# Kernel tuning notes

Hardware: AMD Instinct MI355X
Metric: run time of the kernel (lower is better)

## Reference

```python
import jax, jax.numpy as jnp
import numpy as np

SIGMAS = (1.0, 10.0, 100.0, 1000.0)
EPS_RATIO = 1e-3  # lambda ridge term and ratio clip epsilon


def euclidsq(x, y):
    # squared pairwise Euclidean distances, [m, n]
    d = jnp.sum(x * x, axis=-1)[:, None] + jnp.sum(y * y, axis=-1)[None, :] - 2.0 * (x @ y.T)
    return jnp.maximum(d, 0.0)


def kmm_ratio(Kdede, Kdenu, lam):
    # original: inv(Kdede + lam*I) @ Kdenu @ ones == solve(A, Kdenu @ ones)
    n_de = Kdede.shape[0]
    A = Kdede + lam * jnp.eye(n_de, dtype=Kdede.dtype)
    B = jnp.sum(Kdenu, axis=1, keepdims=True)  # [n_de, 1]
    return jnp.linalg.solve(A, B)


def estimate_ratio(x_de, x_nu):
    # averaged KMM ratio over Gaussian kernels with fixed sigmas, then clip
    dsq_dede = euclidsq(x_de, x_de)
    dsq_denu = euclidsq(x_de, x_nu)
    ratio = 0.0
    for s in SIGMAS:
        inv2s2 = 1.0 / (2.0 * s * s)
        Kdede = jnp.exp(-dsq_dede * inv2s2)
        Kdenu = jnp.exp(-dsq_denu * inv2s2)
        ratio = ratio + kmm_ratio(Kdede, Kdenu, EPS_RATIO)
    ratio = ratio / len(SIGMAS)
    return jax.nn.relu(ratio) + EPS_RATIO  # clip_ratio=True


def reference(z1, z2, perm1, perm2):
    n, d = z1.shape
    z1s, z2s = z1[perm1], z2[perm2]
    # numerator ratio over full concatenated embeddings
    num_ratio = estimate_ratio(jnp.concatenate([z1, z2], axis=-1),
                               jnp.concatenate([z1s, z2s], axis=-1))
    num_ratio = 1.0 / num_ratio  # [n, 1]
    x_nu = jnp.concatenate([z2, z2], axis=-1)  # constant across samples

    def per_sample(z1_i):
        # x_de row j = concat(z1_i, z2_shuffled[j])
        x_de = jnp.concatenate([jnp.broadcast_to(z1_i, (n, d)), z2s], axis=-1)
        return jnp.sum(estimate_ratio(x_de, x_nu))

    denum_sums = jax.vmap(per_sample)(z1)  # [n]
    loss = jnp.sum(-jnp.log(num_ratio[:, 0] / denum_sums))
    return loss


def setup_inputs() -> dict:
    key = jax.random.key(0)
    k1, k2 = jax.random.split(key)
    n, d = 256, 128
    z1 = jax.random.normal(k1, (n, d), dtype=jnp.float32)
    z2 = jax.random.normal(k2, (n, d), dtype=jnp.float32)
    perm1 = jnp.arange(n, dtype=jnp.int32)
    perm2 = jnp.arange(n, dtype=jnp.int32)
    return {"z1": z1, "z2": z2, "perm1": perm1, "perm2": perm2}
```

## Files before the change

### kernel.cpp

```cpp
#include <hip/hip_runtime.h>
#include <math.h>

#define N 256
#define Dd 128

__device__ __forceinline__ double inv2s2_of(int s){
    return (s==0)?0.5:(s==1)?5.0e-3:(s==2)?5.0e-5:5.0e-7;
}

__device__ __forceinline__ void sweep32(double P[32][33], int tid){
    if (tid < 64){
        int r = tid & 31, cg = tid >> 5;
        for (int j = 0; j < 32; j++){
            double d    = P[j][j];
            double invd = 1.0 / d;
            double cr   = P[r][j];
            double s    = cr * invd;
            bool rj = (r == j);
            double nv[16];
            #pragma unroll
            for (int c = 0; c < 16; c++){
                int col = cg*16 + c;
                double pj = P[j][col];
                double v  = P[r][col];
                nv[c] = rj ? ((col == j) ? -invd : v * invd)
                           : ((col == j) ? s : v - s*pj);
            }
            #pragma unroll
            for (int c = 0; c < 16; c++) P[r][cg*16+c] = nv[c];
        }
        #pragma unroll
        for (int c = 0; c < 16; c++) P[r][cg*16+c] = -P[r][cg*16+c];
    }
}

__global__ void k_dist(const float* __restrict__ z1, const float* __restrict__ z2,
                       const int* __restrict__ p1, const int* __restrict__ p2,
                       double* __restrict__ S0, float* __restrict__ M4,
                       float* __restrict__ U4, double* __restrict__ bpart){
    __shared__ float Xs[16][17], Ys[16][17];
    int w = blockIdx.z;
    int tx = threadIdx.x, ty = threadIdx.y;
    int row = blockIdx.y*16 + ty, col = blockIdx.x*16 + tx;
    const float *Xb[2], *Yb[2]; const int *Xp[2], *Yp[2]; int npair = 1;
    Xb[1]=0; Yb[1]=0; Xp[0]=0; Yp[0]=0; Xp[1]=0; Yp[1]=0;
    switch(w){
        case 0: Xb[0]=z1; Yb[0]=z1; Xb[1]=z2; Yb[1]=z2; npair=2; break;
        case 1: Xb[0]=z1; Yb[0]=z1; Yp[0]=p1; Xb[1]=z2; Yb[1]=z2; Yp[1]=p2; npair=2; break;
        case 2: Xb[0]=z2; Yb[0]=z2; Xp[0]=p2; Yp[0]=p2; break;
        case 3: Xb[0]=z2; Yb[0]=z2; Xp[0]=p2; break;
        default:Xb[0]=z1; Yb[0]=z2; break;
    }
    double acc = 0.0;
    for (int p = 0; p < npair; p++){
        const float* X = Xb[p]; const float* Y = Yb[p];
        int xr = blockIdx.y*16 + ty; if (Xp[p]) xr = Xp[p][xr];
        int yr = blockIdx.x*16 + ty; if (Yp[p]) yr = Yp[p][yr];
        for (int c = 0; c < Dd; c += 16){
            __syncthreads();
            Xs[ty][tx] = X[xr*Dd + c + tx];
            Ys[ty][tx] = Y[yr*Dd + c + tx];
            __syncthreads();
            #pragma unroll
            for (int t = 0; t < 16; t++){
                float d = Xs[ty][t] - Ys[tx][t];
                acc += (double)d * (double)d;
            }
        }
    }
    int o = row*N + col;
    if (w == 0){
        #pragma unroll
        for (int s = 0; s < 4; s++){
            double v = exp(-inv2s2_of(s)*acc);
            if (row == col) v += 1.0e-3;
            S0[(size_t)(4+s)*N*N + o] = v;
        }
    } else if (w == 1){
        #pragma unroll
        for (int s = 0; s < 4; s++){
            double v = exp(-inv2s2_of(s)*acc);
            v += __shfl_down(v, 8, 16);
            v += __shfl_down(v, 4, 16);
            v += __shfl_down(v, 2, 16);
            v += __shfl_down(v, 1, 16);
            if (tx == 0) bpart[((size_t)s*N + row)*16 + blockIdx.x] = v;
        }
    } else if (w == 2){
        #pragma unroll
        for (int s = 0; s < 4; s++){
            double v = exp(-inv2s2_of(s)*acc);
            if (row == col) v += 1.0e-3;
            S0[(size_t)s*N*N + o] = v;
        }
    } else if (w == 3){
        #pragma unroll
        for (int s = 0; s < 4; s++) M4[s*N*N + o] = (float)exp(-inv2s2_of(s)*acc);
    } else {
        #pragma unroll
        for (int s = 0; s < 4; s++) U4[s*N*N + o] = (float)exp(-inv2s2_of(s)*acc);
    }
}

__global__ void k_gemm_nt(const float* __restrict__ M4, const float* __restrict__ U4,
                          double* __restrict__ Bmat, const double* __restrict__ S0,
                          double* __restrict__ Pg0, double* __restrict__ dsum){
    __shared__ float Ms[32][33], Us[32][33];
    __shared__ double P[32][33];
    int tx = threadIdx.x, ty = threadIdx.y;
    int tid = ty*16 + tx;
    if (blockIdx.z == 4){
        if (blockIdx.y != 0) return;
        int mat = blockIdx.x;
        if (mat == 0) dsum[tid] = 0.0;
        const double* S = S0 + (size_t)mat*65536;
        #pragma unroll
        for (int l = 0; l < 4; l++){
            int e = tid + l*256; P[e>>5][e&31] = S[(size_t)(e>>5)*N + (e&31)];
        }
        __syncthreads();
        sweep32(P, tid);
        __syncthreads();
        double* Pp = Pg0 + (size_t)mat*1024;
        #pragma unroll
        for (int l = 0; l < 4; l++){
            int e = tid + l*256; Pp[e] = P[e>>5][e&31];
        }
        return;
    }
    int s = blockIdx.z;
    const float* Mp = M4 + s*N*N;
    const float* Up = U4 + s*N*N;
    double* Bp = Bmat + s*N*N;
    int bj = blockIdx.y*32, bi = blockIdx.x*32;
    double a00=0, a01=0, a10=0, a11=0;
    for (int kc = 0; kc < N; kc += 32){
        __syncthreads();
        #pragma unroll
        for (int l = 0; l < 4; l++){
            int e = tid + l*256; int r = e >> 5, c = e & 31;
            Ms[r][c] = Mp[(bj+r)*N + kc + c];
            Us[r][c] = Up[(bi+r)*N + kc + c];
        }
        __syncthreads();
        #pragma unroll
        for (int k = 0; k < 32; k++){
            float x0 = Ms[2*ty][k], x1 = Ms[2*ty+1][k];
            float y0 = Us[2*tx][k], y1 = Us[2*tx+1][k];
            a00 += (double)x0*y0; a01 += (double)x0*y1;
            a10 += (double)x1*y0; a11 += (double)x1*y1;
        }
    }
    Bp[(bj+2*ty  )*N + bi+2*tx  ] = a00;
    Bp[(bj+2*ty  )*N + bi+2*tx+1] = a01;
    Bp[(bj+2*ty+1)*N + bi+2*tx  ] = a10;
    Bp[(bj+2*ty+1)*N + bi+2*tx+1] = a11;
}

__global__ void k_step(const double* __restrict__ Ssrc, double* __restrict__ Sdst,
                       const double* __restrict__ PgS, double* __restrict__ PgD, int k){
    __shared__ double Pl[32][33], EJ[32][33], Cl[32][33], El[32][33];
    int b = blockIdx.x;
    int mat = b & 7;
    int bx = b >> 3;
    const double* S = Ssrc + (size_t)mat*65536;
    double* D = Sdst + (size_t)mat*65536;
    const double* Pp = PgS + (size_t)mat*1024;
    int tid = threadIdx.x;
    int Kb = k*32;
    #pragma unroll
    for (int l = 0; l < 4; l++){
        int e = tid + l*256; Pl[e>>5][e&31] = Pp[e];
    }
    if (bx < 49){
        int I = bx / 7, J = bx % 7;
        int GI = ((I < k) ? I : I + 1) * 32;
        int GJ = ((J < k) ? J : J + 1) * 32;
        #pragma unroll
        for (int l = 0; l < 4; l++){
            int e = tid + l*256; int r = e >> 5, c = e & 31;
            El[r][c] = S[(size_t)(GI + r)*N + Kb + c];
            EJ[r][c] = S[(size_t)(GJ + r)*N + Kb + c];
        }
        __syncthreads();
        #pragma unroll
        for (int l = 0; l < 4; l++){
            int e = tid + l*256; int r = e >> 5, c = e & 31;
            double acc = 0.0;
            #pragma unroll
            for (int kk = 0; kk < 32; kk++) acc += EJ[r][kk] * Pl[kk][c];
            Cl[r][c] = acc;
        }
        __syncthreads();
        int pr = tid >> 4, pc = tid & 15;
        int r0 = 2*pr, c0 = 2*pc;
        double a00 = S[(size_t)(GI+r0)*N + GJ+c0];
        double a01 = S[(size_t)(GI+r0)*N + GJ+c0+1];
        double a10 = S[(size_t)(GI+r0+1)*N + GJ+c0];
        double a11 = S[(size_t)(GI+r0+1)*N + GJ+c0+1];
        #pragma unroll
        for (int kk = 0; kk < 32; kk++){
            double e0 = El[r0][kk],   e1 = El[r0+1][kk];
            double b0 = Cl[c0][kk],   b1 = Cl[c0+1][kk];
            a00 -= e0*b0; a01 -= e0*b1;
            a10 -= e1*b0; a11 -= e1*b1;
        }
        double* Dp = D + (size_t)(GI + r0)*N + GJ + c0;
        Dp[0]   = a00; Dp[1]   = a01;
        Dp[N]   = a10; Dp[N+1] = a11;
        if (I == k && J == k && k < 7){
            __syncthreads();
            El[r0][c0]   = a00; El[r0][c0+1]   = a01;
            El[r0+1][c0] = a10; El[r0+1][c0+1] = a11;
            __syncthreads();
            sweep32(El, tid);
            __syncthreads();
            double* Pd = PgD + (size_t)mat*1024;
            #pragma unroll
            for (int l = 0; l < 4; l++){
                int e = tid + l*256; Pd[e] = El[e>>5][e&31];
            }
        }
    } else {
        int T = bx - 49;
        int GT = ((T < k) ? T : T + 1) * 32;
        #pragma unroll
        for (int l = 0; l < 4; l++){
            int e = tid + l*256; int r = e >> 5, c = e & 31;
            El[r][c] = S[(size_t)(GT + r)*N + Kb + c];
        }
        __syncthreads();
        #pragma unroll
        for (int l = 0; l < 4; l++){
            int e = tid + l*256; int r = e >> 5, c = e & 31;
            double acc = 0.0;
            #pragma unroll
            for (int kk = 0; kk < 32; kk++) acc += El[r][kk] * Pl[kk][c];
            Cl[r][c] = acc;
        }
        __syncthreads();
        #pragma unroll
        for (int l = 0; l < 4; l++){
            int e = tid + l*256; int r = e >> 5, c = e & 31;
            D[(size_t)(GT + r)*N + Kb + c] = Cl[r][c];
        }
        #pragma unroll
        for (int l = 0; l < 4; l++){
            int e = tid + l*256; int cc = e >> 5, rr = e & 31;
            D[(size_t)(Kb + cc)*N + GT + rr] = Cl[rr][cc];
        }
        if (T == 0){
            #pragma unroll
            for (int l = 0; l < 4; l++){
                int e = tid + l*256; int i = e >> 5, j = e & 31;
                D[(size_t)(Kb + i)*N + Kb + j] = -Pl[i][j];
            }
        }
    }
}

__global__ void k_x(const double* __restrict__ Sfin, const double* __restrict__ Bmat,
                    float* __restrict__ Xm){
    int s = blockIdx.z;
    const double* Sp = Sfin + (size_t)s*N*N;
    const double* Bp = Bmat + (size_t)s*N*N;
    float* Xp = Xm + (size_t)s*N*N;
    __shared__ double Gs[32][33], Bs[32][33];
    int tx = threadIdx.x, ty = threadIdx.y;
    int tid = ty*16 + tx;
    int bj = blockIdx.y*32, bi = blockIdx.x*32;
    double a00=0, a01=0, a10=0, a11=0;
    for (int kc = 0; kc < N; kc += 32){
        __syncthreads();
        #pragma unroll
        for (int l = 0; l < 4; l++){
            int e = tid + l*256; int r = e >> 5, c = e & 31;
            Gs[r][c] = -Sp[(size_t)(bj+r)*N + kc + c];
            Bs[r][c] = Bp[(size_t)(kc+r)*N + bi + c];
        }
        __syncthreads();
        #pragma unroll
        for (int k = 0; k < 32; k++){
            double x0 = Gs[2*ty][k], x1 = Gs[2*ty+1][k];
            double y0 = Bs[k][2*tx], y1 = Bs[k][2*tx+1];
            a00 += x0*y0; a01 += x0*y1;
            a10 += x1*y0; a11 += x1*y1;
        }
    }
    Xp[(bj+2*ty  )*N + bi+2*tx  ] = (float)a00;
    Xp[(bj+2*ty  )*N + bi+2*tx+1] = (float)a01;
    Xp[(bj+2*ty+1)*N + bi+2*tx  ] = (float)a10;
    Xp[(bj+2*ty+1)*N + bi+2*tx+1] = (float)a11;
}

__global__ void k_red(const float* __restrict__ Xm, const double* __restrict__ Sfin,
                      const double* __restrict__ bpart, double* __restrict__ dsum,
                      float* __restrict__ rnum){
    __shared__ double cp[32][33];
    __shared__ double bsh[256];
    int b = blockIdx.x, tid = threadIdx.x;
    if (b < 64){
        int bj = (b >> 3)*32, bi = (b & 7)*32;
        #pragma unroll
        for (int l = 0; l < 4; l++){
            int e = tid + l*256; int r = e >> 5, c = e & 31;
            int o = (bj + r)*N + bi + c;
            float x = Xm[0*N*N + o] + Xm[1*N*N + o] + Xm[2*N*N + o] + Xm[3*N*N + o];
            cp[r][c] = (double)fmaxf(0.25f*x, 0.f);
        }
        __syncthreads();
        if (tid < 32){
            double ssum = 0;
            #pragma unroll
            for (int r = 0; r < 32; r++) ssum += cp[r][tid];
            atomicAdd(&dsum[bi + tid], ssum);
        }
    } else {
        int s = b - 64, j = tid;
        const double* Sn = Sfin + (size_t)(4+s)*N*N;
        const double* bp = bpart + (size_t)s*N*16;
        double acc = 0;
        #pragma unroll
        for (int t = 0; t < 16; t++) acc += bp[j*16 + t];
        bsh[j] = acc;
        __syncthreads();
        double y = 0;
        for (int k = 0; k < N; k++) y -= Sn[(size_t)k*N + j] * bsh[k];
        rnum[s*N + j] = (float)y;
    }
}

__global__ void k_loss2(const double* __restrict__ dsum, const float* __restrict__ rnum,
                        float* __restrict__ out){
    __shared__ double red[256];
    int i = threadIdx.x;
    double denum = dsum[i] + (double)N * 1.0e-3;
    float ravg = 0.25f*(rnum[0*N+i] + rnum[1*N+i] + rnum[2*N+i] + rnum[3*N+i]);
    double rn = (double)fmaxf(ravg, 0.f) + 1.0e-3;
    red[i] = log(rn) + log(denum);
    __syncthreads();
    for (int st = 128; st > 0; st >>= 1){
        if (i < st) red[i] += red[i + st];
        __syncthreads();
    }
    if (i == 0) out[0] = (float)red[0];
}

extern "C" void kernel_launch(void* const* d_in, const int* in_sizes, int n_in,
                              void* d_out, int out_size, void* d_ws, size_t ws_size,
                              hipStream_t stream) {
    (void)in_sizes; (void)n_in; (void)out_size; (void)ws_size;
    const float* z1 = (const float*)d_in[0];
    const float* z2 = (const float*)d_in[1];
    const int*   p1 = (const int*)d_in[2];
    const int*   p2 = (const int*)d_in[3];
    float* out = (float*)d_out;

    char* w = (char*)d_ws;
    size_t o = 0;
    auto carve = [&](size_t bytes) -> char* {
        char* p = w + o;
        o += (bytes + 255) & ~(size_t)255;
        return p;
    };
    double* bpart = (double*)carve((size_t)4*N*16*sizeof(double));
    double* dsum  = (double*)carve((size_t)N*sizeof(double));
    float*  M4    = (float*) carve((size_t)4*N*N*sizeof(float));
    float*  U4    = (float*) carve((size_t)4*N*N*sizeof(float));
    double* Bmat  = (double*)carve((size_t)4*N*N*sizeof(double));
    float*  Xm    = (float*) carve((size_t)4*N*N*sizeof(float));
    float*  rnum  = (float*) carve((size_t)4*N*sizeof(float));
    double* S0    = (double*)carve((size_t)8*N*N*sizeof(double));
    double* S1    = (double*)carve((size_t)8*N*N*sizeof(double));
    double* Pg0   = (double*)carve((size_t)8*32*32*sizeof(double));
    double* Pg1   = (double*)carve((size_t)8*32*32*sizeof(double));

    k_dist<<<dim3(16,16,5), dim3(16,16), 0, stream>>>(z1, z2, p1, p2,
                                                      S0, M4, U4, bpart);
    k_gemm_nt<<<dim3(8,8,5), dim3(16,16), 0, stream>>>(M4, U4, Bmat, S0, Pg0, dsum);
    for (int k = 0; k < 8; k++){
        double* src = (k & 1) ? S1 : S0;
        double* dst = (k & 1) ? S0 : S1;
        double* ps  = (k & 1) ? Pg1 : Pg0;
        double* pd  = (k & 1) ? Pg0 : Pg1;
        k_step<<<dim3(448), dim3(256), 0, stream>>>(src, dst, ps, pd, k);
    }
    k_x<<<dim3(8,8,4), dim3(16,16), 0, stream>>>(S0, Bmat, Xm);
    k_red<<<dim3(68), dim3(256), 0, stream>>>(Xm, S0, bpart, dsum, rnum);
    k_loss2<<<dim3(1), dim3(256), 0, stream>>>(dsum, rnum, out);
}
```

Before: 439.7 us.

## Use 64-wide pivot blocks in blocked Gauss-Jordan inversion to halve step launches

The blocked in-place matrix inversion now uses 64x64 pivot blocks instead of 32x32, so the sweep runs 4 step launches instead of 8. Each pivot block is inverted by a two-stage 32-wide sweep inside shared memory (inv64). The step kernel uses larger 4x4 register tiles per thread. The aim is to cut launch count and global traffic per step, at the cost of only 96 blocks per launch (less parallelism) and a longer serial pivot inversion.

```diff
diff --git a/kernel.cpp b/kernel.cpp
--- a/kernel.cpp
+++ b/kernel.cpp
@@ -8,7 +8,7 @@
     return (s==0)?0.5:(s==1)?5.0e-3:(s==2)?5.0e-5:5.0e-7;
 }
 
-__device__ __forceinline__ void sweep32(double P[32][33], int tid){
+__device__ __forceinline__ void sweep32(double (*P)[33], int tid){
     if (tid < 64){
         int r = tid & 31, cg = tid >> 5;
         for (int j = 0; j < 32; j++){
@@ -31,6 +31,48 @@
         }
         #pragma unroll
         for (int c = 0; c < 16; c++) P[r][cg*16+c] = -P[r][cg*16+c];
+    }
+}
+
+__device__ void inv64(double* T, double (*P32)[33], double* C32, int tid){
+    for (int s2 = 0; s2 < 2; s2++){
+        int pb = s2*32, er = 32 - pb;
+        #pragma unroll
+        for (int l = 0; l < 4; l++){
+            int e = tid + l*256;
+            P32[e>>5][e&31] = T[(pb + (e>>5))*65 + pb + (e&31)];
+        }
+        __syncthreads();
+        sweep32(P32, tid);
+        __syncthreads();
+        #pragma unroll
+        for (int l = 0; l < 4; l++){
+            int e = tid + l*256; int r = e>>5, c = e&31;
+            double acc = 0.0;
+            #pragma unroll
+            for (int kk = 0; kk < 32; kk++)
+                acc += T[(er+r)*65 + pb+kk] * P32[kk][c];
+            C32[r*33 + c] = acc;
+        }
+        __syncthreads();
+        #pragma unroll
+        for (int l = 0; l < 4; l++){
+            int e = tid + l*256; int r = e>>5, c = e&31;
+            double acc = T[(er+r)*65 + er+c];
+            #pragma unroll
+            for (int m = 0; m < 32; m++)
+                acc -= T[(er+r)*65 + pb+m] * C32[c*33+m];
+            T[(er+r)*65 + er+c] = acc;
+        }
+        __syncthreads();
+        #pragma unroll
+        for (int l = 0; l < 4; l++){
+            int e = tid + l*256; int r = e>>5, c = e&31;
+            T[(er+r)*65 + pb+c] = C32[r*33+c];
+            T[(pb+r)*65 + er+c] = C32[c*33+r];
+            T[(pb+r)*65 + pb+c] = -P32[r][c];
+        }
+        __syncthreads();
     }
 }
 
@@ -105,8 +147,7 @@
 __global__ void k_gemm_nt(const float* __restrict__ M4, const float* __restrict__ U4,
                           double* __restrict__ Bmat, const double* __restrict__ S0,
                           double* __restrict__ Pg0, double* __restrict__ dsum){
-    __shared__ float Ms[32][33], Us[32][33];
-    __shared__ double P[32][33];
+    __shared__ double pool2[6272];
     int tx = threadIdx.x, ty = threadIdx.y;
     int tid = ty*16 + tx;
     if (blockIdx.z == 4){
@@ -114,20 +155,26 @@
         int mat = blockIdx.x;
         if (mat == 0) dsum[tid] = 0.0;
         const double* S = S0 + (size_t)mat*65536;
-        #pragma unroll
-        for (int l = 0; l < 4; l++){
-            int e = tid + l*256; P[e>>5][e&31] = S[(size_t)(e>>5)*N + (e&31)];
-        }
-        __syncthreads();
-        sweep32(P, tid);
-        __syncthreads();
-        double* Pp = Pg0 + (size_t)mat*1024;
-        #pragma unroll
-        for (int l = 0; l < 4; l++){
-            int e = tid + l*256; Pp[e] = P[e>>5][e&31];
+        double* T = pool2;
+        double (*P32)[33] = (double(*)[33])(pool2 + 4160);
+        double* C32 = pool2 + 5216;
+        #pragma unroll
+        for (int l = 0; l < 16; l++){
+            int e = tid + l*256;
+            T[(e>>6)*65 + (e&63)] = S[(size_t)(e>>6)*N + (e&63)];
+        }
+        __syncthreads();
+        inv64(T, P32, C32, tid);
+        double* Pd = Pg0 + (size_t)mat*4096;
+        #pragma unroll
+        for (int l = 0; l < 16; l++){
+            int e = tid + l*256;
+            Pd[e] = -T[(e>>6)*65 + (e&63)];
         }
         return;
     }
+    float* Ms = (float*)pool2;
+    float* Us = Ms + 1056;
     int s = blockIdx.z;
     const float* Mp = M4 + s*N*N;
     const float* Up = U4 + s*N*N;
@@ -139,14 +186,14 @@
         #pragma unroll
         for (int l = 0; l < 4; l++){
             int e = tid + l*256; int r = e >> 5, c = e & 31;
-            Ms[r][c] = Mp[(bj+r)*N + kc + c];
-            Us[r][c] = Up[(bi+r)*N + kc + c];
+            Ms[r*33+c] = Mp[(bj+r)*N + kc + c];
+            Us[r*33+c] = Up[(bi+r)*N + kc + c];
         }
         __syncthreads();
         #pragma unroll
         for (int k = 0; k < 32; k++){
-            float x0 = Ms[2*ty][k], x1 = Ms[2*ty+1][k];
-            float y0 = Us[2*tx][k], y1 = Us[2*tx+1][k];
+            float x0 = Ms[(2*ty)*33+k], x1 = Ms[(2*ty+1)*33+k];
+            float y0 = Us[(2*tx)*33+k], y1 = Us[(2*tx+1)*33+k];
             a00 += (double)x0*y0; a01 += (double)x0*y1;
             a10 += (double)x1*y0; a11 += (double)x1*y1;
         }
@@ -157,103 +204,160 @@
     Bp[(bj+2*ty+1)*N + bi+2*tx+1] = a11;
 }
 
-__global__ void k_step(const double* __restrict__ Ssrc, double* __restrict__ Sdst,
-                       const double* __restrict__ PgS, double* __restrict__ PgD, int k){
-    __shared__ double Pl[32][33], EJ[32][33], Cl[32][33], El[32][33];
+__launch_bounds__(256, 2)
+__global__ void k_step64(const double* __restrict__ Ssrc, double* __restrict__ Sdst,
+                         const double* __restrict__ PgS, double* __restrict__ PgD, int k){
+    __shared__ double pool[6400];
+    double* A  = pool;
+    double* B  = pool + 2112;
+    double* Cb = pool + 4160;
     int b = blockIdx.x;
     int mat = b & 7;
-    int bx = b >> 3;
+    int t = b >> 3;
     const double* S = Ssrc + (size_t)mat*65536;
     double* D = Sdst + (size_t)mat*65536;
-    const double* Pp = PgS + (size_t)mat*1024;
+    const double* Pp = PgS + (size_t)mat*4096;
     int tid = threadIdx.x;
-    int Kb = k*32;
-    #pragma unroll
-    for (int l = 0; l < 4; l++){
-        int e = tid + l*256; Pl[e>>5][e&31] = Pp[e];
-    }
-    if (bx < 49){
-        int I = bx / 7, J = bx % 7;
-        int GI = ((I < k) ? I : I + 1) * 32;
-        int GJ = ((J < k) ? J : J + 1) * 32;
-        #pragma unroll
-        for (int l = 0; l < 4; l++){
-            int e = tid + l*256; int r = e >> 5, c = e & 31;
-            El[r][c] = S[(size_t)(GI + r)*N + Kb + c];
-            EJ[r][c] = S[(size_t)(GJ + r)*N + Kb + c];
-        }
-        __syncthreads();
-        #pragma unroll
-        for (int l = 0; l < 4; l++){
-            int e = tid + l*256; int r = e >> 5, c = e & 31;
-            double acc = 0.0;
-            #pragma unroll
-            for (int kk = 0; kk < 32; kk++) acc += EJ[r][kk] * Pl[kk][c];
-            Cl[r][c] = acc;
-        }
-        __syncthreads();
-        int pr = tid >> 4, pc = tid & 15;
-        int r0 = 2*pr, c0 = 2*pc;
-        double a00 = S[(size_t)(GI+r0)*N + GJ+c0];
-        double a01 = S[(size_t)(GI+r0)*N + GJ+c0+1];
-        double a10 = S[(size_t)(GI+r0+1)*N + GJ+c0];
-        double a11 = S[(size_t)(GI+r0+1)*N + GJ+c0+1];
-        #pragma unroll
-        for (int kk = 0; kk < 32; kk++){
-            double e0 = El[r0][kk],   e1 = El[r0+1][kk];
-            double b0 = Cl[c0][kk],   b1 = Cl[c0+1][kk];
-            a00 -= e0*b0; a01 -= e0*b1;
-            a10 -= e1*b0; a11 -= e1*b1;
-        }
-        double* Dp = D + (size_t)(GI + r0)*N + GJ + c0;
-        Dp[0]   = a00; Dp[1]   = a01;
-        Dp[N]   = a10; Dp[N+1] = a11;
-        if (I == k && J == k && k < 7){
-            __syncthreads();
-            El[r0][c0]   = a00; El[r0][c0+1]   = a01;
-            El[r0+1][c0] = a10; El[r0+1][c0+1] = a11;
-            __syncthreads();
-            sweep32(El, tid);
-            __syncthreads();
-            double* Pd = PgD + (size_t)mat*1024;
-            #pragma unroll
-            for (int l = 0; l < 4; l++){
-                int e = tid + l*256; Pd[e] = El[e>>5][e&31];
+    int Kb = k*64;
+    int rg = tid & 31, cg = tid >> 5;
+    if (t < 9){
+        int I = t/3, J = t%3;
+        int GI = ((I<k)?I:I+1)*64, GJ = ((J<k)?J:J+1)*64;
+        int pr = tid>>4, pc = tid&15;
+        double facc[4][4];
+        #pragma unroll
+        for (int i = 0; i < 4; i++)
+            #pragma unroll
+            for (int j = 0; j < 4; j++)
+                facc[i][j] = S[(size_t)(GI+4*pr+i)*N + GJ + pc + 16*j];
+        for (int h = 0; h < 2; h++){
+            double cacc[2][4] = {{0,0,0,0},{0,0,0,0}};
+            __syncthreads();
+            #pragma unroll
+            for (int l = 0; l < 8; l++){
+                int e = tid + l*256;
+                B[e] = Pp[(e>>5)*64 + 32*h + (e&31)];
+            }
+            for (int g = 0; g < 2; g++){
+                #pragma unroll
+                for (int l = 0; l < 8; l++){
+                    int e = tid + l*256;
+                    A[(e>>5)*33 + (e&31)] = S[(size_t)(GJ + (e>>5))*N + Kb + 32*g + (e&31)];
+                }
+                __syncthreads();
+                for (int mm = 0; mm < 32; mm++){
+                    double a0 = A[rg*33 + mm];
+                    double a1 = A[(rg+32)*33 + mm];
+                    #pragma unroll
+                    for (int j = 0; j < 4; j++){
+                        double bb = B[(32*g+mm)*32 + cg*4 + j];
+                        cacc[0][j] += a0*bb;
+                        cacc[1][j] += a1*bb;
+                    }
+                }
+                __syncthreads();
+            }
+            #pragma unroll
+            for (int i = 0; i < 2; i++)
+                #pragma unroll
+                for (int j = 0; j < 4; j++)
+                    Cb[(rg+32*i)*35 + cg*4 + j] = cacc[i][j];
+            __syncthreads();
+            #pragma unroll
+            for (int l = 0; l < 8; l++){
+                int e = tid + l*256;
+                A[(e>>5)*33 + (e&31)] = S[(size_t)(GI + (e>>5))*N + Kb + 32*h + (e&31)];
+            }
+            __syncthreads();
+            for (int mm = 0; mm < 32; mm++){
+                double ei[4], cj[4];
+                #pragma unroll
+                for (int i = 0; i < 4; i++) ei[i] = A[(4*pr+i)*33 + mm];
+                #pragma unroll
+                for (int j = 0; j < 4; j++) cj[j] = Cb[(pc+16*j)*35 + mm];
+                #pragma unroll
+                for (int i = 0; i < 4; i++)
+                    #pragma unroll
+                    for (int j = 0; j < 4; j++)
+                        facc[i][j] -= ei[i]*cj[j];
+            }
+        }
+        #pragma unroll
+        for (int i = 0; i < 4; i++)
+            #pragma unroll
+            for (int j = 0; j < 4; j++)
+                D[(size_t)(GI+4*pr+i)*N + GJ + pc + 16*j] = facc[i][j];
+        if (I == k && J == k && k < 3){
+            double* T = pool;
+            double (*P32)[33] = (double(*)[33])(pool + 4160);
+            double* C32 = pool + 5216;
+            __syncthreads();
+            #pragma unroll
+            for (int i = 0; i < 4; i++)
+                #pragma unroll
+                for (int j = 0; j < 4; j++)
+                    T[(4*pr+i)*65 + pc + 16*j] = facc[i][j];
+            __syncthreads();
+            inv64(T, P32, C32, tid);
+            double* Pd = PgD + (size_t)mat*4096;
+            #pragma unroll
+            for (int l = 0; l < 16; l++){
+                int e = tid + l*256;
+                Pd[e] = -T[(e>>6)*65 + (e&63)];
             }
         }
     } else {
-        int T = bx - 49;
-        int GT = ((T < k) ? T : T + 1) * 32;
-        #pragma unroll
-        for (int l = 0; l < 4; l++){
-            int e = tid + l*256; int r = e >> 5, c = e & 31;
-            El[r][c] = S[(size_t)(GT + r)*N + Kb + c];
-        }
-        __syncthreads();
-        #pragma unroll
-        for (int l = 0; l < 4; l++){
-            int e = tid + l*256; int r = e >> 5, c = e & 31;
-            double acc = 0.0;
-            #pragma unroll
-            for (int kk = 0; kk < 32; kk++) acc += El[r][kk] * Pl[kk][c];
-            Cl[r][c] = acc;
-        }
-        __syncthreads();
-        #pragma unroll
-        for (int l = 0; l < 4; l++){
-            int e = tid + l*256; int r = e >> 5, c = e & 31;
-            D[(size_t)(GT + r)*N + Kb + c] = Cl[r][c];
-        }
-        #pragma unroll
-        for (int l = 0; l < 4; l++){
-            int e = tid + l*256; int cc = e >> 5, rr = e & 31;
-            D[(size_t)(Kb + cc)*N + GT + rr] = Cl[rr][cc];
-        }
-        if (T == 0){
-            #pragma unroll
-            for (int l = 0; l < 4; l++){
-                int e = tid + l*256; int i = e >> 5, j = e & 31;
-                D[(size_t)(Kb + i)*N + Kb + j] = -Pl[i][j];
+        int T_ = t - 9;
+        int GT = ((T_<k)?T_:T_+1)*64;
+        for (int h = 0; h < 2; h++){
+            double cacc[2][4] = {{0,0,0,0},{0,0,0,0}};
+            __syncthreads();
+            #pragma unroll
+            for (int l = 0; l < 8; l++){
+                int e = tid + l*256;
+                B[e] = Pp[(e>>5)*64 + 32*h + (e&31)];
+            }
+            for (int g = 0; g < 2; g++){
+                #pragma unroll
+                for (int l = 0; l < 8; l++){
+                    int e = tid + l*256;
+                    A[(e>>5)*33 + (e&31)] = S[(size_t)(GT + (e>>5))*N + Kb + 32*g + (e&31)];
+                }
+                __syncthreads();
+                for (int mm = 0; mm < 32; mm++){
+                    double a0 = A[rg*33 + mm];
+                    double a1 = A[(rg+32)*33 + mm];
+                    #pragma unroll
+                    for (int j = 0; j < 4; j++){
+                        double bb = B[(32*g+mm)*32 + cg*4 + j];
+                        cacc[0][j] += a0*bb;
+                        cacc[1][j] += a1*bb;
+                    }
+                }
+                __syncthreads();
+            }
+            #pragma unroll
+            for (int i = 0; i < 2; i++)
+                #pragma unroll
+                for (int j = 0; j < 4; j++)
+                    Cb[(rg+32*i)*35 + cg*4 + j] = cacc[i][j];
+            __syncthreads();
+            #pragma unroll
+            for (int l = 0; l < 8; l++){
+                int e = tid + l*256; int r = e>>5, c = e&31;
+                D[(size_t)(GT+r)*N + Kb + 32*h + c] = Cb[r*35 + c];
+            }
+            #pragma unroll
+            for (int l = 0; l < 8; l++){
+                int e = tid + l*256; int cl = e>>6, rr = e&63;
+                D[(size_t)(Kb + 32*h + cl)*N + GT + rr] = Cb[rr*35 + cl];
+            }
+        }
+        if (T_ == 0){
+            #pragma unroll
+            for (int l = 0; l < 16; l++){
+                int e = tid + l*256;
+                D[(size_t)(Kb + (e>>6))*N + Kb + (e&63)] = -Pp[e];
             }
         }
     }
@@ -372,18 +476,18 @@
     float*  rnum  = (float*) carve((size_t)4*N*sizeof(float));
     double* S0    = (double*)carve((size_t)8*N*N*sizeof(double));
     double* S1    = (double*)carve((size_t)8*N*N*sizeof(double));
-    double* Pg0   = (double*)carve((size_t)8*32*32*sizeof(double));
-    double* Pg1   = (double*)carve((size_t)8*32*32*sizeof(double));
+    double* Pg0   = (double*)carve((size_t)8*64*64*sizeof(double));
+    double* Pg1   = (double*)carve((size_t)8*64*64*sizeof(double));
 
     k_dist<<<dim3(16,16,5), dim3(16,16), 0, stream>>>(z1, z2, p1, p2,
                                                       S0, M4, U4, bpart);
     k_gemm_nt<<<dim3(8,8,5), dim3(16,16), 0, stream>>>(M4, U4, Bmat, S0, Pg0, dsum);
-    for (int k = 0; k < 8; k++){
+    for (int k = 0; k < 4; k++){
         double* src = (k & 1) ? S1 : S0;
         double* dst = (k & 1) ? S0 : S1;
         double* ps  = (k & 1) ? Pg1 : Pg0;
         double* pd  = (k & 1) ? Pg0 : Pg1;
-        k_step<<<dim3(448), dim3(256), 0, stream>>>(src, dst, ps, pd, k);
+        k_step64<<<dim3(96), dim3(256), 0, stream>>>(src, dst, ps, pd, k);
     }
     k_x<<<dim3(8,8,4), dim3(16,16), 0, stream>>>(S0, Bmat, Xm);
     k_red<<<dim3(68), dim3(256), 0, stream>>>(Xm, S0, bpart, dsum, rnum);
```

After: 637.4 us. 1.45x slower.

## Exploit symmetry in sweep inversion to update only lower-triangular tiles

Applied to the files above, without the earlier changes.

The symmetric kernel matrices and their in-place sweep inverse are now stored and updated only in the lower block triangle. k_step launches 28 lower tiles plus 7 panel tiles per matrix instead of 49+7, and reads upper-triangle panels through transposed loads. k_x and k_red reconstruct the full matrix from the lower half, and k_dist skips writing the upper tiles. This cuts the FLOPs and memory traffic of the 8 step kernels at the cost of strided transposed global loads and a slightly uneven triangular index computation.

```diff
diff --git a/kernel.cpp b/kernel.cpp
--- a/kernel.cpp
+++ b/kernel.cpp
@@ -8,7 +8,7 @@
     return (s==0)?0.5:(s==1)?5.0e-3:(s==2)?5.0e-5:5.0e-7;
 }
 
-__device__ __forceinline__ void sweep32(double P[32][33], int tid){
+__device__ __forceinline__ void sweep32(double (*P)[33], int tid){
     if (tid < 64){
         int r = tid & 31, cg = tid >> 5;
         for (int j = 0; j < 32; j++){
@@ -69,12 +69,15 @@
         }
     }
     int o = row*N + col;
+    bool lowerTile = (row >> 5) >= (col >> 5);
     if (w == 0){
-        #pragma unroll
-        for (int s = 0; s < 4; s++){
-            double v = exp(-inv2s2_of(s)*acc);
-            if (row == col) v += 1.0e-3;
-            S0[(size_t)(4+s)*N*N + o] = v;
+        if (lowerTile){
+            #pragma unroll
+            for (int s = 0; s < 4; s++){
+                double v = exp(-inv2s2_of(s)*acc);
+                if (row == col) v += 1.0e-3;
+                S0[(size_t)(4+s)*N*N + o] = v;
+            }
         }
     } else if (w == 1){
         #pragma unroll
@@ -87,11 +90,13 @@
             if (tx == 0) bpart[((size_t)s*N + row)*16 + blockIdx.x] = v;
         }
     } else if (w == 2){
-        #pragma unroll
-        for (int s = 0; s < 4; s++){
-            double v = exp(-inv2s2_of(s)*acc);
-            if (row == col) v += 1.0e-3;
-            S0[(size_t)s*N*N + o] = v;
+        if (lowerTile){
+            #pragma unroll
+            for (int s = 0; s < 4; s++){
+                double v = exp(-inv2s2_of(s)*acc);
+                if (row == col) v += 1.0e-3;
+                S0[(size_t)s*N*N + o] = v;
+            }
         }
     } else if (w == 3){
         #pragma unroll
@@ -162,7 +167,7 @@
     __shared__ double Pl[32][33], EJ[32][33], Cl[32][33], El[32][33];
     int b = blockIdx.x;
     int mat = b & 7;
-    int bx = b >> 3;
+    int t = b >> 3;
     const double* S = Ssrc + (size_t)mat*65536;
     double* D = Sdst + (size_t)mat*65536;
     const double* Pp = PgS + (size_t)mat*1024;
@@ -172,16 +177,28 @@
     for (int l = 0; l < 4; l++){
         int e = tid + l*256; Pl[e>>5][e&31] = Pp[e];
     }
-    if (bx < 49){
-        int I = bx / 7, J = bx % 7;
+    auto loadE = [&](double (*buf)[33], int Gx){
+        if (Gx > Kb){
+            #pragma unroll
+            for (int l = 0; l < 4; l++){
+                int e = tid + l*256; int r = e >> 5, c = e & 31;
+                buf[r][c] = S[(size_t)(Gx + r)*N + Kb + c];
+            }
+        } else {
+            #pragma unroll
+            for (int l = 0; l < 4; l++){
+                int e = tid + l*256; int a = e >> 5, bb = e & 31;
+                buf[bb][a] = S[(size_t)(Kb + a)*N + Gx + bb];
+            }
+        }
+    };
+    if (t < 28){
+        int I = 0; { int tt = t; while ((I+1)*(I+2)/2 <= tt) I++; }
+        int J = t - I*(I+1)/2;
         int GI = ((I < k) ? I : I + 1) * 32;
         int GJ = ((J < k) ? J : J + 1) * 32;
-        #pragma unroll
-        for (int l = 0; l < 4; l++){
-            int e = tid + l*256; int r = e >> 5, c = e & 31;
-            El[r][c] = S[(size_t)(GI + r)*N + Kb + c];
-            EJ[r][c] = S[(size_t)(GJ + r)*N + Kb + c];
-        }
+        loadE(El, GI);
+        loadE(EJ, GJ);
         __syncthreads();
         #pragma unroll
         for (int l = 0; l < 4; l++){
@@ -222,13 +239,9 @@
             }
         }
     } else {
-        int T = bx - 49;
-        int GT = ((T < k) ? T : T + 1) * 32;
-        #pragma unroll
-        for (int l = 0; l < 4; l++){
-            int e = tid + l*256; int r = e >> 5, c = e & 31;
-            El[r][c] = S[(size_t)(GT + r)*N + Kb + c];
-        }
+        int i = t - 28;
+        int Gi = ((i < k) ? i : i + 1) * 32;
+        loadE(El, Gi);
         __syncthreads();
         #pragma unroll
         for (int l = 0; l < 4; l++){
@@ -239,21 +252,24 @@
             Cl[r][c] = acc;
         }
         __syncthreads();
-        #pragma unroll
-        for (int l = 0; l < 4; l++){
-            int e = tid + l*256; int r = e >> 5, c = e & 31;
-            D[(size_t)(GT + r)*N + Kb + c] = Cl[r][c];
-        }
-        #pragma unroll
-        for (int l = 0; l < 4; l++){
-            int e = tid + l*256; int cc = e >> 5, rr = e & 31;
-            D[(size_t)(Kb + cc)*N + GT + rr] = Cl[rr][cc];
-        }
-        if (T == 0){
-            #pragma unroll
-            for (int l = 0; l < 4; l++){
-                int e = tid + l*256; int i = e >> 5, j = e & 31;
-                D[(size_t)(Kb + i)*N + Kb + j] = -Pl[i][j];
+        if (Gi > Kb){
+            #pragma unroll
+            for (int l = 0; l < 4; l++){
+                int e = tid + l*256; int r = e >> 5, c = e & 31;
+                D[(size_t)(Gi + r)*N + Kb + c] = Cl[r][c];
+            }
+        } else {
+            #pragma unroll
+            for (int l = 0; l < 4; l++){
+                int e = tid + l*256; int r = e >> 5, c = e & 31;
+                D[(size_t)(Kb + r)*N + Gi + c] = Cl[c][r];
+            }
+        }
+        if (i == 0){
+            #pragma unroll
+            for (int l = 0; l < 4; l++){
+                int e = tid + l*256; int r = e >> 5, c = e & 31;
+                D[(size_t)(Kb + r)*N + Kb + c] = -Pl[r][c];
             }
         }
     }
@@ -272,11 +288,20 @@
     double a00=0, a01=0, a10=0, a11=0;
     for (int kc = 0; kc < N; kc += 32){
         __syncthreads();
-        #pragma unroll
-        for (int l = 0; l < 4; l++){
-            int e = tid + l*256; int r = e >> 5, c = e & 31;
-            Gs[r][c] = -Sp[(size_t)(bj+r)*N + kc + c];
-            Bs[r][c] = Bp[(size_t)(kc+r)*N + bi + c];
+        if (bj >= kc){
+            #pragma unroll
+            for (int l = 0; l < 4; l++){
+                int e = tid + l*256; int r = e >> 5, c = e & 31;
+                Gs[r][c] = -Sp[(size_t)(bj+r)*N + kc + c];
+                Bs[r][c] = Bp[(size_t)(kc+r)*N + bi + c];
+            }
+        } else {
+            #pragma unroll
+            for (int l = 0; l < 4; l++){
+                int e = tid + l*256; int a = e >> 5, bb = e & 31;
+                Gs[bb][a] = -Sp[(size_t)(kc+a)*N + bj + bb];
+                Bs[a][bb] = Bp[(size_t)(kc+a)*N + bi + bb];
+            }
         }
         __syncthreads();
         #pragma unroll
@@ -325,7 +350,8 @@
         bsh[j] = acc;
         __syncthreads();
         double y = 0;
-        for (int k = 0; k < N; k++) y -= Sn[(size_t)k*N + j] * bsh[k];
+        for (int k = 0; k < j; k++)   y -= Sn[(size_t)j*N + k] * bsh[k];
+        for (int k = j; k < N; k++)   y -= Sn[(size_t)k*N + j] * bsh[k];
         rnum[s*N + j] = (float)y;
     }
 }
@@ -383,7 +409,7 @@
         double* dst = (k & 1) ? S0 : S1;
         double* ps  = (k & 1) ? Pg1 : Pg0;
         double* pd  = (k & 1) ? Pg0 : Pg1;
-        k_step<<<dim3(448), dim3(256), 0, stream>>>(src, dst, ps, pd, k);
+        k_step<<<dim3(280), dim3(256), 0, stream>>>(src, dst, ps, pd, k);
     }
     k_x<<<dim3(8,8,4), dim3(16,16), 0, stream>>>(S0, Bmat, Xm);
     k_red<<<dim3(68), dim3(256), 0, stream>>>(Xm, S0, bpart, dsum, rnum);
```

Result: slower. 453.0 us (+3.0%).

## Use 64-wide pivot blocks in block Gauss-Jordan inversion and fuse X/reduction kernels

Applied to the files above, without the earlier changes.

Raises the pivot block size of the blocked sweep inversion from 32 to 64, halving the number of step launches from eight to four. Each 64x64 pivot is inverted by two 32-wide sub-sweeps in a new inv64 routine. The first pivot moves to its own kernel, and later pivots are formed inside the step by dedicated blocks. The separate X GEMM and reduction kernels are merged so the four sigma products are summed in registers, dropping the Xm buffer. In exchange, the serial pivot blocks do more work per step and some blocks run longer.

```diff
diff --git a/kernel.cpp b/kernel.cpp
--- a/kernel.cpp
+++ b/kernel.cpp
@@ -8,7 +8,7 @@
     return (s==0)?0.5:(s==1)?5.0e-3:(s==2)?5.0e-5:5.0e-7;
 }
 
-__device__ __forceinline__ void sweep32(double P[32][33], int tid){
+__device__ __forceinline__ void sweep32(double (*P)[33], int tid){
     if (tid < 64){
         int r = tid & 31, cg = tid >> 5;
         for (int j = 0; j < 32; j++){
@@ -31,6 +31,48 @@
         }
         #pragma unroll
         for (int c = 0; c < 16; c++) P[r][cg*16+c] = -P[r][cg*16+c];
+    }
+}
+
+__device__ void inv64(double* T, double (*P32)[33], double* C32, int tid){
+    for (int s2 = 0; s2 < 2; s2++){
+        int pb = s2*32, er = 32 - pb;
+        #pragma unroll
+        for (int l = 0; l < 4; l++){
+            int e = tid + l*256;
+            P32[e>>5][e&31] = T[(pb + (e>>5))*66 + pb + (e&31)];
+        }
+        __syncthreads();
+        sweep32(P32, tid);
+        __syncthreads();
+        #pragma unroll
+        for (int l = 0; l < 4; l++){
+            int e = tid + l*256; int r = e>>5, c = e&31;
+            double acc = 0.0;
+            #pragma unroll
+            for (int kk = 0; kk < 32; kk++)
+                acc += T[(er+r)*66 + pb+kk] * P32[kk][c];
+            C32[r*33 + c] = acc;
+        }
+        __syncthreads();
+        #pragma unroll
+        for (int l = 0; l < 4; l++){
+            int e = tid + l*256; int r = e>>5, c = e&31;
+            double acc = T[(er+r)*66 + er+c];
+            #pragma unroll
+            for (int m = 0; m < 32; m++)
+                acc -= T[(er+r)*66 + pb+m] * C32[c*33+m];
+            T[(er+r)*66 + er+c] = acc;
+        }
+        __syncthreads();
+        #pragma unroll
+        for (int l = 0; l < 4; l++){
+            int e = tid + l*256; int r = e>>5, c = e&31;
+            T[(er+r)*66 + pb+c] = C32[r*33+c];
+            T[(pb+r)*66 + er+c] = C32[c*33+r];
+            T[(pb+r)*66 + pb+c] = -P32[r][c];
+        }
+        __syncthreads();
     }
 }
 
@@ -103,31 +145,10 @@
 }
 
 __global__ void k_gemm_nt(const float* __restrict__ M4, const float* __restrict__ U4,
-                          double* __restrict__ Bmat, const double* __restrict__ S0,
-                          double* __restrict__ Pg0, double* __restrict__ dsum){
+                          double* __restrict__ Bmat){
     __shared__ float Ms[32][33], Us[32][33];
-    __shared__ double P[32][33];
     int tx = threadIdx.x, ty = threadIdx.y;
     int tid = ty*16 + tx;
-    if (blockIdx.z == 4){
-        if (blockIdx.y != 0) return;
-        int mat = blockIdx.x;
-        if (mat == 0) dsum[tid] = 0.0;
-        const double* S = S0 + (size_t)mat*65536;
-        #pragma unroll
-        for (int l = 0; l < 4; l++){
-            int e = tid + l*256; P[e>>5][e&31] = S[(size_t)(e>>5)*N + (e&31)];
-        }
-        __syncthreads();
-        sweep32(P, tid);
-        __syncthreads();
-        double* Pp = Pg0 + (size_t)mat*1024;
-        #pragma unroll
-        for (int l = 0; l < 4; l++){
-            int e = tid + l*256; Pp[e] = P[e>>5][e&31];
-        }
-        return;
-    }
     int s = blockIdx.z;
     const float* Mp = M4 + s*N*N;
     const float* Up = U4 + s*N*N;
@@ -157,166 +178,225 @@
     Bp[(bj+2*ty+1)*N + bi+2*tx+1] = a11;
 }
 
-__global__ void k_step(const double* __restrict__ Ssrc, double* __restrict__ Sdst,
-                       const double* __restrict__ PgS, double* __restrict__ PgD, int k){
-    __shared__ double Pl[32][33], EJ[32][33], Cl[32][33], El[32][33];
+__global__ void k_piv0(const double* __restrict__ S0, double* __restrict__ Pg0,
+                       double* __restrict__ dsum){
+    __shared__ double pool[6336];
+    double* T = pool;
+    double (*P32)[33] = (double(*)[33])(pool + 4224);
+    double* C32 = pool + 5280;
+    int mat = blockIdx.x, tid = threadIdx.x;
+    if (mat == 0) dsum[tid] = 0.0;
+    const double* S = S0 + (size_t)mat*65536;
+    #pragma unroll
+    for (int l = 0; l < 16; l++){
+        int e = tid + l*256;
+        T[(e>>6)*66 + (e&63)] = S[(size_t)(e>>6)*N + (e&63)];
+    }
+    __syncthreads();
+    inv64(T, P32, C32, tid);
+    double* Pd = Pg0 + (size_t)mat*4096;
+    #pragma unroll
+    for (int l = 0; l < 16; l++){
+        int e = tid + l*256;
+        Pd[e] = -T[(e>>6)*66 + (e&63)];
+    }
+}
+
+__global__ void k_step64(const double* __restrict__ Ssrc, double* __restrict__ Sdst,
+                         const double* __restrict__ PgS, double* __restrict__ PgD, int k){
+    __shared__ double pool[6336];
+    double (*Pl)[33] = (double(*)[33])(pool);
+    double (*EJ)[33] = (double(*)[33])(pool + 1056);
+    double (*Cl)[33] = (double(*)[33])(pool + 2112);
+    double (*El)[33] = (double(*)[33])(pool + 3168);
+    double* T = pool;
+    double (*P32)[33] = (double(*)[33])(pool + 4224);
+    double* C32 = pool + 5280;
     int b = blockIdx.x;
     int mat = b & 7;
-    int bx = b >> 3;
+    int t = b >> 3;
     const double* S = Ssrc + (size_t)mat*65536;
     double* D = Sdst + (size_t)mat*65536;
-    const double* Pp = PgS + (size_t)mat*1024;
+    const double* Pp = PgS + (size_t)mat*4096;
     int tid = threadIdx.x;
-    int Kb = k*32;
-    #pragma unroll
-    for (int l = 0; l < 4; l++){
-        int e = tid + l*256; Pl[e>>5][e&31] = Pp[e];
-    }
-    if (bx < 49){
-        int I = bx / 7, J = bx % 7;
-        int GI = ((I < k) ? I : I + 1) * 32;
-        int GJ = ((J < k) ? J : J + 1) * 32;
+    int Kb = k*64;
+    int pr = tid >> 4, pc = tid & 15;
+    int r0 = 2*pr, c0 = 2*pc;
+    auto stageS = [&](double (*buf)[33], int rb, int cb){
         #pragma unroll
         for (int l = 0; l < 4; l++){
             int e = tid + l*256; int r = e >> 5, c = e & 31;
-            El[r][c] = S[(size_t)(GI + r)*N + Kb + c];
-            EJ[r][c] = S[(size_t)(GJ + r)*N + Kb + c];
-        }
-        __syncthreads();
+            buf[r][c] = S[(size_t)(rb + r)*N + cb + c];
+        }
+    };
+    auto stageP = [&](double (*buf)[33], int h, int m){
         #pragma unroll
         for (int l = 0; l < 4; l++){
             int e = tid + l*256; int r = e >> 5, c = e & 31;
-            double acc = 0.0;
-            #pragma unroll
-            for (int kk = 0; kk < 32; kk++) acc += EJ[r][kk] * Pl[kk][c];
-            Cl[r][c] = acc;
-        }
-        __syncthreads();
-        int pr = tid >> 4, pc = tid & 15;
-        int r0 = 2*pr, c0 = 2*pc;
-        double a00 = S[(size_t)(GI+r0)*N + GJ+c0];
-        double a01 = S[(size_t)(GI+r0)*N + GJ+c0+1];
-        double a10 = S[(size_t)(GI+r0+1)*N + GJ+c0];
-        double a11 = S[(size_t)(GI+r0+1)*N + GJ+c0+1];
-        #pragma unroll
-        for (int kk = 0; kk < 32; kk++){
-            double e0 = El[r0][kk],   e1 = El[r0+1][kk];
-            double b0 = Cl[c0][kk],   b1 = Cl[c0+1][kk];
-            a00 -= e0*b0; a01 -= e0*b1;
-            a10 -= e1*b0; a11 -= e1*b1;
+            buf[r][c] = Pp[(h*32 + r)*64 + m*32 + c];
+        }
+    };
+    auto fmap = [&](int i){ return ((i < k) ? i : i + 1) * 64; };
+
+    if (t < 36){
+        int q = t >> 2, sub = t & 3;
+        int I = q / 3, J = q % 3;
+        int a = sub >> 1, b2 = sub & 1;
+        int GI = fmap(I) + a*32, GJ = fmap(J) + b2*32;
+        double f00 = S[(size_t)(GI+r0)*N + GJ+c0];
+        double f01 = S[(size_t)(GI+r0)*N + GJ+c0+1];
+        double f10 = S[(size_t)(GI+r0+1)*N + GJ+c0];
+        double f11 = S[(size_t)(GI+r0+1)*N + GJ+c0+1];
+        for (int m = 0; m < 2; m++){
+            double ce[4] = {0,0,0,0};
+            for (int h = 0; h < 2; h++){
+                __syncthreads();
+                stageS(EJ, fmap(J) + b2*32, Kb + h*32);
+                stageP(Pl, h, m);
+                __syncthreads();
+                #pragma unroll
+                for (int l = 0; l < 4; l++){
+                    int e = tid + l*256; int r = e >> 5, c = e & 31;
+                    double acc = 0.0;
+                    #pragma unroll
+                    for (int kk = 0; kk < 32; kk++) acc += EJ[r][kk] * Pl[kk][c];
+                    ce[l] += acc;
+                }
+            }
+            __syncthreads();
+            #pragma unroll
+            for (int l = 0; l < 4; l++){
+                int e = tid + l*256; Cl[e>>5][e&31] = ce[l];
+            }
+            stageS(El, fmap(I) + a*32, Kb + m*32);
+            __syncthreads();
+            #pragma unroll
+            for (int kk = 0; kk < 32; kk++){
+                double e0 = El[r0][kk],   e1 = El[r0+1][kk];
+                double b0 = Cl[c0][kk],   b1 = Cl[c0+1][kk];
+                f00 -= e0*b0; f01 -= e0*b1;
+                f10 -= e1*b0; f11 -= e1*b1;
+            }
         }
         double* Dp = D + (size_t)(GI + r0)*N + GJ + c0;
-        Dp[0]   = a00; Dp[1]   = a01;
-        Dp[N]   = a10; Dp[N+1] = a11;
-        if (I == k && J == k && k < 7){
-            __syncthreads();
-            El[r0][c0]   = a00; El[r0][c0+1]   = a01;
-            El[r0+1][c0] = a10; El[r0+1][c0+1] = a11;
-            __syncthreads();
-            sweep32(El, tid);
-            __syncthreads();
-            double* Pd = PgD + (size_t)mat*1024;
+        Dp[0] = f00; Dp[1] = f01; Dp[N] = f10; Dp[N+1] = f11;
+    } else if (t < 48){
+        int tt = t - 36;
+        int i = tt >> 2, sub = tt & 3;
+        int a = sub >> 1, b2 = sub & 1;
+        int Gi = fmap(i);
+        double ce[4] = {0,0,0,0};
+        for (int h = 0; h < 2; h++){
+            __syncthreads();
+            stageS(EJ, Gi + a*32, Kb + h*32);
+            stageP(Pl, h, b2);
+            __syncthreads();
             #pragma unroll
             for (int l = 0; l < 4; l++){
-                int e = tid + l*256; Pd[e] = El[e>>5][e&31];
-            }
+                int e = tid + l*256; int r = e >> 5, c = e & 31;
+                double acc = 0.0;
+                #pragma unroll
+                for (int kk = 0; kk < 32; kk++) acc += EJ[r][kk] * Pl[kk][c];
+                ce[l] += acc;
+            }
+        }
+        __syncthreads();
+        #pragma unroll
+        for (int l = 0; l < 4; l++){
+            int e = tid + l*256; Cl[e>>5][e&31] = ce[l];
+        }
+        __syncthreads();
+        #pragma unroll
+        for (int l = 0; l < 4; l++){
+            int e = tid + l*256; int r = e >> 5, c = e & 31;
+            D[(size_t)(Gi + a*32 + r)*N + Kb + b2*32 + c] = Cl[r][c];
+        }
+        #pragma unroll
+        for (int l = 0; l < 4; l++){
+            int e = tid + l*256; int cc = e >> 5, rr = e & 31;
+            D[(size_t)(Kb + b2*32 + cc)*N + Gi + a*32 + rr] = Cl[rr][cc];
+        }
+    } else if (t < 52){
+        int sub = t - 48;
+        int a = sub >> 1, b2 = sub & 1;
+        #pragma unroll
+        for (int l = 0; l < 4; l++){
+            int e = tid + l*256; int r = e >> 5, c = e & 31;
+            D[(size_t)(Kb + a*32 + r)*N + Kb + b2*32 + c] = -Pp[(a*32 + r)*64 + b2*32 + c];
         }
     } else {
-        int T = bx - 49;
-        int GT = ((T < k) ? T : T + 1) * 32;
-        #pragma unroll
-        for (int l = 0; l < 4; l++){
-            int e = tid + l*256; int r = e >> 5, c = e & 31;
-            El[r][c] = S[(size_t)(GT + r)*N + Kb + c];
-        }
-        __syncthreads();
-        #pragma unroll
-        for (int l = 0; l < 4; l++){
-            int e = tid + l*256; int r = e >> 5, c = e & 31;
-            double acc = 0.0;
-            #pragma unroll
-            for (int kk = 0; kk < 32; kk++) acc += El[r][kk] * Pl[kk][c];
-            Cl[r][c] = acc;
-        }
-        __syncthreads();
-        #pragma unroll
-        for (int l = 0; l < 4; l++){
-            int e = tid + l*256; int r = e >> 5, c = e & 31;
-            D[(size_t)(GT + r)*N + Kb + c] = Cl[r][c];
-        }
-        #pragma unroll
-        for (int l = 0; l < 4; l++){
-            int e = tid + l*256; int cc = e >> 5, rr = e & 31;
-            D[(size_t)(Kb + cc)*N + GT + rr] = Cl[rr][cc];
-        }
-        if (T == 0){
-            #pragma unroll
-            for (int l = 0; l < 4; l++){
-                int e = tid + l*256; int i = e >> 5, j = e & 31;
-                D[(size_t)(Kb + i)*N + Kb + j] = -Pl[i][j];
-            }
-        }
-    }
-}
-
-__global__ void k_x(const double* __restrict__ Sfin, const double* __restrict__ Bmat,
-                    float* __restrict__ Xm){
-    int s = blockIdx.z;
-    const double* Sp = Sfin + (size_t)s*N*N;
-    const double* Bp = Bmat + (size_t)s*N*N;
-    float* Xp = Xm + (size_t)s*N*N;
+        if (k >= 3) return;
+        int GIb = fmap(k);
+        double fac[4][4];
+        for (int sub = 0; sub < 4; sub++){
+            int a = sub >> 1, b2 = sub & 1;
+            int GI = GIb + a*32, GJ = GIb + b2*32;
+            fac[sub][0] = S[(size_t)(GI+r0)*N + GJ+c0];
+            fac[sub][1] = S[(size_t)(GI+r0)*N + GJ+c0+1];
+            fac[sub][2] = S[(size_t)(GI+r0+1)*N + GJ+c0];
+            fac[sub][3] = S[(size_t)(GI+r0+1)*N + GJ+c0+1];
+            for (int m = 0; m < 2; m++){
+                double ce[4] = {0,0,0,0};
+                for (int h = 0; h < 2; h++){
+                    __syncthreads();
+                    stageS(EJ, GIb + b2*32, Kb + h*32);
+                    stageP(Pl, h, m);
+                    __syncthreads();
+                    #pragma unroll
+                    for (int l = 0; l < 4; l++){
+                        int e = tid + l*256; int r = e >> 5, c = e & 31;
+                        double acc = 0.0;
+                        #pragma unroll
+                        for (int kk = 0; kk < 32; kk++) acc += EJ[r][kk] * Pl[kk][c];
+                        ce[l] += acc;
+                    }
+                }
+                __syncthreads();
+                #pragma unroll
+                for (int l = 0; l < 4; l++){
+                    int e = tid + l*256; Cl[e>>5][e&31] = ce[l];
+                }
+                stageS(El, GIb + a*32, Kb + m*32);
+                __syncthreads();
+                #pragma unroll
+                for (int kk = 0; kk < 32; kk++){
+                    double e0 = El[r0][kk],   e1 = El[r0+1][kk];
+                    double b0 = Cl[c0][kk],   b1 = Cl[c0+1][kk];
+                    fac[sub][0] -= e0*b0; fac[sub][1] -= e0*b1;
+                    fac[sub][2] -= e1*b0; fac[sub][3] -= e1*b1;
+                }
+                __syncthreads();
+            }
+        }
+        for (int sub = 0; sub < 4; sub++){
+            int a = sub >> 1, b2 = sub & 1;
+            T[(a*32+r0  )*66 + b2*32+c0  ] = fac[sub][0];
+            T[(a*32+r0  )*66 + b2*32+c0+1] = fac[sub][1];
+            T[(a*32+r0+1)*66 + b2*32+c0  ] = fac[sub][2];
+            T[(a*32+r0+1)*66 + b2*32+c0+1] = fac[sub][3];
+        }
+        __syncthreads();
+        inv64(T, P32, C32, tid);
+        double* Pd = PgD + (size_t)mat*4096;
+        #pragma unroll
+        for (int l = 0; l < 16; l++){
+            int e = tid + l*256;
+            Pd[e] = -T[(e>>6)*66 + (e&63)];
+        }
+    }
+}
+
+__global__ void k_xl(const double* __restrict__ Sfin, const double* __restrict__ Bmat,
+                     double* __restrict__ dsum, const double* __restrict__ bpart,
+                     float* __restrict__ rnum){
     __shared__ double Gs[32][33], Bs[32][33];
+    __shared__ double cp[16][33];
+    __shared__ double bsh[256];
     int tx = threadIdx.x, ty = threadIdx.y;
     int tid = ty*16 + tx;
-    int bj = blockIdx.y*32, bi = blockIdx.x*32;
-    double a00=0, a01=0, a10=0, a11=0;
-    for (int kc = 0; kc < N; kc += 32){
-        __syncthreads();
-        #pragma unroll
-        for (int l = 0; l < 4; l++){
-            int e = tid + l*256; int r = e >> 5, c = e & 31;
-            Gs[r][c] = -Sp[(size_t)(bj+r)*N + kc + c];
-            Bs[r][c] = Bp[(size_t)(kc+r)*N + bi + c];
-        }
-        __syncthreads();
-        #pragma unroll
-        for (int k = 0; k < 32; k++){
-            double x0 = Gs[2*ty][k], x1 = Gs[2*ty+1][k];
-            double y0 = Bs[k][2*tx], y1 = Bs[k][2*tx+1];
-            a00 += x0*y0; a01 += x0*y1;
-            a10 += x1*y0; a11 += x1*y1;
-        }
-    }
-    Xp[(bj+2*ty  )*N + bi+2*tx  ] = (float)a00;
-    Xp[(bj+2*ty  )*N + bi+2*tx+1] = (float)a01;
-    Xp[(bj+2*ty+1)*N + bi+2*tx  ] = (float)a10;
-    Xp[(bj+2*ty+1)*N + bi+2*tx+1] = (float)a11;
-}
-
-__global__ void k_red(const float* __restrict__ Xm, const double* __restrict__ Sfin,
-                      const double* __restrict__ bpart, double* __restrict__ dsum,
-                      float* __restrict__ rnum){
-    __shared__ double cp[32][33];
-    __shared__ double bsh[256];
-    int b = blockIdx.x, tid = threadIdx.x;
-    if (b < 64){
-        int bj = (b >> 3)*32, bi = (b & 7)*32;
-        #pragma unroll
-        for (int l = 0; l < 4; l++){
-            int e = tid + l*256; int r = e >> 5, c = e & 31;
-            int o = (bj + r)*N + bi + c;
-            float x = Xm[0*N*N + o] + Xm[1*N*N + o] + Xm[2*N*N + o] + Xm[3*N*N + o];
-            cp[r][c] = (double)fmaxf(0.25f*x, 0.f);
-        }
-        __syncthreads();
-        if (tid < 32){
-            double ssum = 0;
-            #pragma unroll
-            for (int r = 0; r < 32; r++) ssum += cp[r][tid];
-            atomicAdd(&dsum[bi + tid], ssum);
-        }
-    } else {
-        int s = b - 64, j = tid;
+    if (blockIdx.y == 8){
+        if (blockIdx.x >= 4) return;
+        int s = blockIdx.x, j = tid;
         const double* Sn = Sfin + (size_t)(4+s)*N*N;
         const double* bp = bpart + (size_t)s*N*16;
         double acc = 0;
@@ -327,6 +407,47 @@
         double y = 0;
         for (int k = 0; k < N; k++) y -= Sn[(size_t)k*N + j] * bsh[k];
         rnum[s*N + j] = (float)y;
+        return;
+    }
+    int bj = blockIdx.y*32, bi = blockIdx.x*32;
+    int r0 = bj+2*ty, c0 = bi+2*tx;
+    double s00=0, s01=0, s10=0, s11=0;
+    for (int s = 0; s < 4; s++){
+        const double* Sp = Sfin + (size_t)s*N*N;
+        const double* Bp = Bmat + (size_t)s*N*N;
+        double a00=0, a01=0, a10=0, a11=0;
+        for (int kc = 0; kc < N; kc += 32){
+            __syncthreads();
+            #pragma unroll
+            for (int l = 0; l < 4; l++){
+                int e = tid + l*256; int r = e >> 5, c = e & 31;
+                Gs[r][c] = -Sp[(size_t)(bj+r)*N + kc + c];
+                Bs[r][c] = Bp[(size_t)(kc+r)*N + bi + c];
+            }
+            __syncthreads();
+            #pragma unroll
+            for (int k = 0; k < 32; k++){
+                double x0 = Gs[2*ty][k], x1 = Gs[2*ty+1][k];
+                double y0 = Bs[k][2*tx], y1 = Bs[k][2*tx+1];
+                a00 += x0*y0; a01 += x0*y1;
+                a10 += x1*y0; a11 += x1*y1;
+            }
+        }
+        s00 += a00; s01 += a01; s10 += a10; s11 += a11;
+    }
+    double v00 = (double)fmaxf((float)(0.25*s00), 0.f);
+    double v01 = (double)fmaxf((float)(0.25*s01), 0.f);
+    double v10 = (double)fmaxf((float)(0.25*s10), 0.f);
+    double v11 = (double)fmaxf((float)(0.25*s11), 0.f);
+    __syncthreads();
+    cp[ty][2*tx]   = v00 + v10;
+    cp[ty][2*tx+1] = v01 + v11;
+    __syncthreads();
+    if (tid < 32){
+        double ssum = 0;
+        #pragma unroll
+        for (int t = 0; t < 16; t++) ssum += cp[t][tid];
+        atomicAdd(&dsum[bi + tid], ssum);
     }
 }
 
@@ -368,24 +489,23 @@
     float*  M4    = (float*) carve((size_t)4*N*N*sizeof(float));
     float*  U4    = (float*) carve((size_t)4*N*N*sizeof(float));
     double* Bmat  = (double*)carve((size_t)4*N*N*sizeof(double));
-    float*  Xm    = (float*) carve((size_t)4*N*N*sizeof(float));
     float*  rnum  = (float*) carve((size_t)4*N*sizeof(float));
     double* S0    = (double*)carve((size_t)8*N*N*sizeof(double));
     double* S1    = (double*)carve((size_t)8*N*N*sizeof(double));
-    double* Pg0   = (double*)carve((size_t)8*32*32*sizeof(double));
-    double* Pg1   = (double*)carve((size_t)8*32*32*sizeof(double));
+    double* Pg0   = (double*)carve((size_t)8*64*64*sizeof(double));
+    double* Pg1   = (double*)carve((size_t)8*64*64*sizeof(double));
 
     k_dist<<<dim3(16,16,5), dim3(16,16), 0, stream>>>(z1, z2, p1, p2,
                                                       S0, M4, U4, bpart);
-    k_gemm_nt<<<dim3(8,8,5), dim3(16,16), 0, stream>>>(M4, U4, Bmat, S0, Pg0, dsum);
-    for (int k = 0; k < 8; k++){
+    k_gemm_nt<<<dim3(8,8,4), dim3(16,16), 0, stream>>>(M4, U4, Bmat);
+    k_piv0<<<dim3(8), dim3(256), 0, stream>>>(S0, Pg0, dsum);
+    for (int k = 0; k < 4; k++){
         double* src = (k & 1) ? S1 : S0;
         double* dst = (k & 1) ? S0 : S1;
         double* ps  = (k & 1) ? Pg1 : Pg0;
         double* pd  = (k & 1) ? Pg0 : Pg1;
-        k_step<<<dim3(448), dim3(256), 0, stream>>>(src, dst, ps, pd, k);
-    }
-    k_x<<<dim3(8,8,4), dim3(16,16), 0, stream>>>(S0, Bmat, Xm);
-    k_red<<<dim3(68), dim3(256), 0, stream>>>(Xm, S0, bpart, dsum, rnum);
+        k_step64<<<dim3(424), dim3(256), 0, stream>>>(src, dst, ps, pd, k);
+    }
+    k_xl<<<dim3(8,9), dim3(16,16), 0, stream>>>(S0, Bmat, dsum, bpart, rnum);
     k_loss2<<<dim3(1), dim3(256), 0, stream>>>(dsum, rnum, out);
 }
```

After: 852.9 us. 1.94x slower.
